# Kernel optimization log

Hardware: AMD Instinct MI355X
Metric: run time of the kernel (lower is better)

The kernel has to match this reference:

```python
import jax, jax.numpy as jnp
import numpy as np

B, T, V, D, OUT = 32, 100, 10000, 128, 1000
CODE_P = 0.003  # ~30 active codes per visit


def gru_dir(x3, whh, bhh, reverse):
    """x3: [B,T,3F] precomputed input-side gates (W_ih x + b_ih). PyTorch GRU math."""
    F = whh.shape[1]
    h0 = jnp.zeros((x3.shape[0], F), x3.dtype)

    def step(h, xt):
        gh = h @ whh.T + bhh
        xr, xz, xn = jnp.split(xt, 3, -1)
        hr, hz, hn = jnp.split(gh, 3, -1)
        r = jax.nn.sigmoid(xr + hr)
        z = jax.nn.sigmoid(xz + hz)
        n = jnp.tanh(xn + r * hn)
        h_new = (1.0 - z) * n + z * h
        return h_new, h_new

    _, hs = jax.lax.scan(step, h0, jnp.swapaxes(x3, 0, 1), reverse=reverse)
    return jnp.swapaxes(hs, 0, 1)  # [B,T,F]


def setup_inputs() -> dict:
    key = jax.random.key(0)
    ks = jax.random.split(key, 16)
    s = lambda k, *sh: jax.random.normal(k, sh, dtype=jnp.float32) * 0.05
    # multi-hot visits, ~0/1 with density CODE_P; force code 0 present so no all-zero visit
    x = (jax.random.uniform(ks[0], (B, T, V)) < CODE_P).astype(jnp.float32)
    x = x.at[:, :, 0].set(1.0)
    return {
        "batchdata": x,
        "emb": s(ks[1], V, D),
        "wih_f": s(ks[2], 3 * D, D), "whh_f": s(ks[3], 3 * D, D),
        "bih_f": jnp.zeros((3 * D,), jnp.float32), "bhh_f": jnp.zeros((3 * D,), jnp.float32),
        "wih_b": s(ks[4], 3 * D, D), "whh_b": s(ks[5], 3 * D, D),
        "bih_b": jnp.zeros((3 * D,), jnp.float32), "bhh_b": jnp.zeros((3 * D,), jnp.float32),
        "attn_w": s(ks[6], 2 * D, 1), "attn_b": jnp.zeros((1,), jnp.float32),
        "comb_w": s(ks[7], D, 4 * D), "comb_b": jnp.zeros((D,), jnp.float32),
        "fc_w": s(ks[8], OUT, D), "fc_b": jnp.zeros((OUT,), jnp.float32),
    }


def reference(batchdata, emb, wih_f, whh_f, bih_f, bhh_f, wih_b, whh_b, bih_b, bhh_b,
              attn_w, attn_b, comb_w, comb_b, fc_w, fc_b):
    # multihot_to_embedding: sum of embedding rows where visit==1 == multihot @ table
    e = jnp.einsum('btv,vd->btd', batchdata, emb)          # [B,T,D]
    mask = jnp.any(e != 0, axis=2)                          # [B,T]
    # DipoleLayer: bidirectional GRU (hidden=D each dir), dropout in eval mode = identity
    xf = jnp.einsum('btf,gf->btg', e, wih_f) + bih_f
    xb = jnp.einsum('btf,gf->btg', e, wih_b) + bih_b
    hf = gru_dir(xf, whh_f, bhh_f, reverse=False)
    hb = gru_dir(xb, whh_b, bhh_b, reverse=True)
    h = jnp.concatenate([hf, hb], axis=-1)                  # [B,T,2D]
    # location-based attention over timesteps
    scores = (h @ attn_w)[..., 0] + attn_b[0]               # [B,T]
    scores = jnp.where(mask, scores, jnp.float32(-1e9))
    a = jax.nn.softmax(scores, axis=-1)
    c = jnp.einsum('bt,btf->bf', a, h)                      # [B,2D] context
    last = jnp.sum(mask.astype(jnp.int32), axis=-1) - 1     # last valid visit
    h_last = h[jnp.arange(h.shape[0]), last]                # [B,2D]
    feat = jnp.tanh(jnp.concatenate([c, h_last], -1) @ comb_w.T + comb_b)  # [B,D]
    logits = feat @ fc_w.T + fc_b                           # [B,OUT]
    return logits
```

## Files before the change

### kernel.cpp

```cpp
#include <hip/hip_runtime.h>
#include <math.h>

#define BB 32
#define TT 100
#define VV 10000
#define DD 128
#define OUTN 1000
#define G3 384

__global__ __launch_bounds__(256) void k_embed(
    const float* __restrict__ x, const float* __restrict__ emb,
    float* __restrict__ e, int* __restrict__ mask)
{
    const int bt  = blockIdx.x;
    const int tid = threadIdx.x;
    __shared__ int   s_cnt;
    __shared__ int   s_any;
    __shared__ int   s_idx[256];
    __shared__ float s_val[256];
    if (tid == 0) { s_cnt = 0; s_any = 0; }
    __syncthreads();

    const float4* x4 = (const float4*)(x + (size_t)bt * VV);
    for (int i = tid; i < VV / 4; i += 256) {
        float4 v = x4[i];
        if (v.x != 0.f) { int p = atomicAdd(&s_cnt, 1); if (p < 256) { s_idx[p] = 4*i+0; s_val[p] = v.x; } }
        if (v.y != 0.f) { int p = atomicAdd(&s_cnt, 1); if (p < 256) { s_idx[p] = 4*i+1; s_val[p] = v.y; } }
        if (v.z != 0.f) { int p = atomicAdd(&s_cnt, 1); if (p < 256) { s_idx[p] = 4*i+2; s_val[p] = v.z; } }
        if (v.w != 0.f) { int p = atomicAdd(&s_cnt, 1); if (p < 256) { s_idx[p] = 4*i+3; s_val[p] = v.w; } }
    }
    __syncthreads();
    int cnt = s_cnt; if (cnt > 256) cnt = 256;
    if (tid < DD) {
        float acc = 0.f;
        for (int i = 0; i < cnt; ++i)
            acc += s_val[i] * emb[(size_t)s_idx[i] * DD + tid];
        e[(size_t)bt * DD + tid] = acc;
        if (acc != 0.f) s_any = 1;
    }
    __syncthreads();
    if (tid == 0) mask[bt] = s_any;
}

__global__ __launch_bounds__(256) void k_gates(
    const float* __restrict__ e,
    const float* __restrict__ wih_f, const float* __restrict__ bih_f,
    const float* __restrict__ wih_b, const float* __restrict__ bih_b,
    float* __restrict__ x3)
{
    const int r0  = blockIdx.x * 8;
    const int tid = threadIdx.x;
    __shared__ __align__(16) float se[8][DD];
    for (int i = tid; i < 8 * DD; i += 256)
        se[i >> 7][i & 127] = e[(size_t)(r0 + (i >> 7)) * DD + (i & 127)];
    __syncthreads();

    for (int cc = 0; cc < 3; ++cc) {
        const int col = tid + cc * 256;
        const float* wrow;
        float bias;
        if (col < G3) { wrow = wih_f + (size_t)col * DD;        bias = bih_f[col]; }
        else          { wrow = wih_b + (size_t)(col - G3) * DD; bias = bih_b[col - G3]; }
        float acc[8];
        #pragma unroll
        for (int r = 0; r < 8; ++r) acc[r] = 0.f;
        const float4* w4 = (const float4*)wrow;
        for (int k4 = 0; k4 < DD / 4; ++k4) {
            float4 w = w4[k4];
            #pragma unroll
            for (int r = 0; r < 8; ++r) {
                float4 ev = *(const float4*)&se[r][4 * k4];
                acc[r] += ev.x * w.x + ev.y * w.y + ev.z * w.z + ev.w * w.w;
            }
        }
        #pragma unroll
        for (int r = 0; r < 8; ++r)
            x3[(size_t)(r0 + r) * 768 + col] = acc[r] + bias;
    }
}

__global__ __launch_bounds__(384, 2) void k_gru(
    const float* __restrict__ x3,
    const float* __restrict__ whh_f, const float* __restrict__ bhh_f,
    const float* __restrict__ whh_b, const float* __restrict__ bhh_b,
    float* __restrict__ h_all)
{
    const int dir = blockIdx.x & 1;
    const int b   = blockIdx.x >> 1;
    const int g   = threadIdx.x;
    const float* whh = dir ? whh_b : whh_f;
    const float* bhh = dir ? bhh_b : bhh_f;

    float4 W[32];
    {
        const float4* wr4 = (const float4*)(whh + (size_t)g * DD);
        #pragma unroll
        for (int j = 0; j < 32; ++j) W[j] = wr4[j];
    }
    const float bh = bhh[g];

    __shared__ __align__(16) float h_lds[DD];
    __shared__ float gh_lds[G3];
    float h_reg = 0.f;
    if (g < DD) h_lds[g] = 0.f;
    __syncthreads();

    for (int t = 0; t < TT; ++t) {
        const int te = dir ? (TT - 1 - t) : t;
        const float* x3p = x3 + (size_t)(b * TT + te) * 768 + dir * G3;
        float xr = 0.f, xz = 0.f, xn = 0.f;
        if (g < DD) { xr = x3p[g]; xz = x3p[DD + g]; xn = x3p[2 * DD + g]; }

        float acc[8];
        #pragma unroll
        for (int i = 0; i < 8; ++i) acc[i] = 0.f;
        #pragma unroll
        for (int j = 0; j < 32; ++j) {
            float4 hv = *(const float4*)&h_lds[4 * j];
            float4 wv = W[j];
            acc[j & 7] += wv.x * hv.x + wv.y * hv.y + wv.z * hv.z + wv.w * hv.w;
        }
        gh_lds[g] = ((acc[0] + acc[1]) + (acc[2] + acc[3]))
                  + ((acc[4] + acc[5]) + (acc[6] + acc[7])) + bh;
        __syncthreads();

        if (g < DD) {
            float hr = gh_lds[g], hz = gh_lds[DD + g], hn = gh_lds[2 * DD + g];
            float r  = __builtin_amdgcn_rcpf(1.f + __expf(-(xr + hr)));
            float z  = __builtin_amdgcn_rcpf(1.f + __expf(-(xz + hz)));
            float e2 = __expf(2.f * (xn + r * hn));
            float n  = 1.f - 2.f * __builtin_amdgcn_rcpf(e2 + 1.f);
            float hnew = n + z * (h_reg - n);
            h_reg = hnew;
            h_lds[g] = hnew;
            h_all[(size_t)((dir * BB + b) * TT + te) * DD + g] = hnew;
        }
        __syncthreads();
    }
}

__global__ __launch_bounds__(256) void k_attn(
    const float* __restrict__ h_all, const int* __restrict__ mask,
    const float* __restrict__ attn_w, const float* __restrict__ attn_b,
    const float* __restrict__ comb_w, const float* __restrict__ comb_b,
    float* __restrict__ feat)
{
    const int b   = blockIdx.x;
    const int tid = threadIdx.x;
    __shared__ float s_aw[256];
    __shared__ float s_sc[128];
    __shared__ int   s_m[128];
    __shared__ float s_red[128];
    __shared__ __align__(16) float s_ch[512];

    s_aw[tid] = attn_w[tid];
    int m = 0;
    if (tid < 128) {
        m = (tid < TT) ? mask[b * TT + tid] : 0;
        s_m[tid] = m;
    }
    __syncthreads();
    for (int s = 64; s > 0; s >>= 1) {
        if (tid < s) s_m[tid] += s_m[tid + s];
        __syncthreads();
    }
    const int last = s_m[0] - 1;

    const float* hf = h_all + (size_t)(0 * BB + b) * TT * DD;
    const float* hb = h_all + (size_t)(1 * BB + b) * TT * DD;

    float sc = -1e9f;
    if (tid < TT) {
        float a = attn_b[0];
        const float4* hf4 = (const float4*)(hf + (size_t)tid * DD);
        const float4* hb4 = (const float4*)(hb + (size_t)tid * DD);
        for (int k = 0; k < DD / 4; ++k) {
            float4 v = hf4[k];
            a += v.x * s_aw[4*k] + v.y * s_aw[4*k+1] + v.z * s_aw[4*k+2] + v.w * s_aw[4*k+3];
        }
        for (int k = 0; k < DD / 4; ++k) {
            float4 v = hb4[k];
            a += v.x * s_aw[DD+4*k] + v.y * s_aw[DD+4*k+1] + v.z * s_aw[DD+4*k+2] + v.w * s_aw[DD+4*k+3];
        }
        sc = m ? a : -1e9f;
    }
    if (tid < 128) { s_sc[tid] = sc; s_red[tid] = sc; }
    __syncthreads();
    for (int s = 64; s > 0; s >>= 1) {
        if (tid < s) s_red[tid] = fmaxf(s_red[tid], s_red[tid + s]);
        __syncthreads();
    }
    const float mx = s_red[0];
    __syncthreads();
    float ex = 0.f;
    if (tid < 128) { ex = __expf(s_sc[tid] - mx); s_sc[tid] = ex; s_red[tid] = ex; }
    __syncthreads();
    for (int s = 64; s > 0; s >>= 1) {
        if (tid < s) s_red[tid] += s_red[tid + s];
        __syncthreads();
    }
    const float inv = 1.f / s_red[0];
    __syncthreads();

    {
        const int fl = tid & 127;
        const float* hp = (tid < 128) ? hf : hb;
        float csum = 0.f;
        for (int t = 0; t < TT; ++t)
            csum += s_sc[t] * hp[(size_t)t * DD + fl];
        s_ch[tid]       = csum * inv;
        s_ch[256 + tid] = hp[(size_t)last * DD + fl];
    }
    __syncthreads();

    if (tid < 128) {
        float a = comb_b[tid];
        const float4* cw = (const float4*)(comb_w + (size_t)tid * 512);
        for (int k = 0; k < 128; ++k) {
            float4 w4 = cw[k];
            float4 v4 = *(const float4*)&s_ch[4 * k];
            a += w4.x * v4.x + w4.y * v4.y + w4.z * v4.z + w4.w * v4.w;
        }
        feat[(size_t)b * DD + tid] = tanhf(a);
    }
}

__global__ __launch_bounds__(256) void k_logits(
    const float* __restrict__ feat, const float* __restrict__ fc_w,
    const float* __restrict__ fc_b, float* __restrict__ out)
{
    const int b   = blockIdx.x >> 2;
    const int oc  = blockIdx.x & 3;
    const int tid = threadIdx.x;
    const int o   = oc * 256 + tid;
    __shared__ __align__(16) float s_f[DD];
    if (tid < DD) s_f[tid] = feat[(size_t)b * DD + tid];
    __syncthreads();
    if (o < OUTN) {
        float a = fc_b[o];
        const float4* w4 = (const float4*)(fc_w + (size_t)o * DD);
        for (int k = 0; k < DD / 4; ++k) {
            float4 w = w4[k];
            float4 v = *(const float4*)&s_f[4 * k];
            a += w.x * v.x + w.y * v.y + w.z * v.z + w.w * v.w;
        }
        out[(size_t)b * OUTN + o] = a;
    }
}

extern "C" void kernel_launch(void* const* d_in, const int* in_sizes, int n_in,
                              void* d_out, int out_size, void* d_ws, size_t ws_size,
                              hipStream_t stream)
{
    const float* x      = (const float*)d_in[0];
    const float* emb    = (const float*)d_in[1];
    const float* wih_f  = (const float*)d_in[2];
    const float* whh_f  = (const float*)d_in[3];
    const float* bih_f  = (const float*)d_in[4];
    const float* bhh_f  = (const float*)d_in[5];
    const float* wih_b  = (const float*)d_in[6];
    const float* whh_b  = (const float*)d_in[7];
    const float* bih_b  = (const float*)d_in[8];
    const float* bhh_b  = (const float*)d_in[9];
    const float* attn_w = (const float*)d_in[10];
    const float* attn_b = (const float*)d_in[11];
    const float* comb_w = (const float*)d_in[12];
    const float* comb_b = (const float*)d_in[13];
    const float* fc_w   = (const float*)d_in[14];
    const float* fc_b   = (const float*)d_in[15];
    float* out = (float*)d_out;

    float* ws    = (float*)d_ws;
    float* e     = ws;
    int*   mask  = (int*)(ws + 409600);
    float* x3    = ws + 412800;
    float* h_all = ws + 2870400;
    float* feat  = ws + 3689600;

    k_embed <<<BB * TT,      256, 0, stream>>>(x, emb, e, mask);
    k_gates <<<(BB * TT)/8,  256, 0, stream>>>(e, wih_f, bih_f, wih_b, bih_b, x3);
    k_gru   <<<2 * BB,       384, 0, stream>>>(x3, whh_f, bhh_f, whh_b, bhh_b, h_all);
    k_attn  <<<BB,           256, 0, stream>>>(h_all, mask, attn_w, attn_b, comb_w, comb_b, feat);
    k_logits<<<BB * 4,       256, 0, stream>>>(feat, fc_w, fc_b, out);
}
```

Measured before the change: 414.4 us.

## Split GRU recurrent matvec by hidden unit and K-half across 256 threads

Reworks the GRU recurrence so each thread owns one hidden unit's r, z and n rows over half of the K dimension, instead of one thread per gate row. Each thread holds 48 float4 weights in registers. The upper half writes its partial sums to LDS and the lower half combines them and applies the gate math locally. This removes the gh_lds gather across gate rows and cuts the block to 256 threads, aiming to shorten the per-step critical path. The cost is higher register pressure (192 floats of weights per thread) and a cross-half partial-sum exchange each step.

```diff
diff --git a/kernel.cpp b/kernel.cpp
--- a/kernel.cpp
+++ b/kernel.cpp
@@ -79,7 +79,7 @@
     }
 }
 
-__global__ __launch_bounds__(384, 2) void k_gru(
+__global__ __launch_bounds__(256, 1) void k_gru(
     const float* __restrict__ x3,
     const float* __restrict__ whh_f, const float* __restrict__ bhh_f,
     const float* __restrict__ whh_b, const float* __restrict__ bhh_b,
@@ -87,45 +87,51 @@
 {
     const int dir = blockIdx.x & 1;
     const int b   = blockIdx.x >> 1;
-    const int g   = threadIdx.x;
+    const int tid = threadIdx.x;
+    const int g   = tid & 127;
+    const int kh  = tid >> 7;
+    const int kb  = kh * 64;
     const float* whh = dir ? whh_b : whh_f;
     const float* bhh = dir ? bhh_b : bhh_f;
 
-    float4 W[32];
-    {
-        const float4* wr4 = (const float4*)(whh + (size_t)g * DD);
-        #pragma unroll
-        for (int j = 0; j < 32; ++j) W[j] = wr4[j];
-    }
-    const float bh = bhh[g];
+    const float4* pr4 = (const float4*)(whh + (size_t)(g         ) * DD + kb);
+    const float4* pz4 = (const float4*)(whh + (size_t)(DD     + g) * DD + kb);
+    const float4* pn4 = (const float4*)(whh + (size_t)(2 * DD + g) * DD + kb);
+
+#define Q16(M) M(0) M(1) M(2) M(3) M(4) M(5) M(6) M(7) M(8) M(9) M(10) M(11) M(12) M(13) M(14) M(15)
+#define DECLW(i) float4 wr##i = pr4[i], wz##i = pz4[i], wn##i = pn4[i];
+    Q16(DECLW)
+
+    const float bhr = bhh[g], bhz = bhh[DD + g], bhn = bhh[2 * DD + g];
 
     __shared__ __align__(16) float h_lds[DD];
-    __shared__ float gh_lds[G3];
+    __shared__ float p_lds[3 * DD];
     float h_reg = 0.f;
-    if (g < DD) h_lds[g] = 0.f;
+    if (tid < DD) h_lds[tid] = 0.f;
     __syncthreads();
 
     for (int t = 0; t < TT; ++t) {
         const int te = dir ? (TT - 1 - t) : t;
         const float* x3p = x3 + (size_t)(b * TT + te) * 768 + dir * G3;
         float xr = 0.f, xz = 0.f, xn = 0.f;
-        if (g < DD) { xr = x3p[g]; xz = x3p[DD + g]; xn = x3p[2 * DD + g]; }
-
-        float acc[8];
-        #pragma unroll
-        for (int i = 0; i < 8; ++i) acc[i] = 0.f;
-        #pragma unroll
-        for (int j = 0; j < 32; ++j) {
-            float4 hv = *(const float4*)&h_lds[4 * j];
-            float4 wv = W[j];
-            acc[j & 7] += wv.x * hv.x + wv.y * hv.y + wv.z * hv.z + wv.w * hv.w;
-        }
-        gh_lds[g] = ((acc[0] + acc[1]) + (acc[2] + acc[3]))
-                  + ((acc[4] + acc[5]) + (acc[6] + acc[7])) + bh;
-        __syncthreads();
-
-        if (g < DD) {
-            float hr = gh_lds[g], hz = gh_lds[DD + g], hn = gh_lds[2 * DD + g];
+        if (tid < DD) { xr = x3p[g]; xz = x3p[DD + g]; xn = x3p[2 * DD + g]; }
+
+        float ar0 = 0.f, ar1 = 0.f, az0 = 0.f, az1 = 0.f, an0 = 0.f, an1 = 0.f;
+#define FMA(i) { float4 hv = *(const float4*)&h_lds[kb + 4 * (i)]; \
+        (((i)&1) ? ar1 : ar0) += wr##i.x*hv.x + wr##i.y*hv.y + wr##i.z*hv.z + wr##i.w*hv.w; \
+        (((i)&1) ? az1 : az0) += wz##i.x*hv.x + wz##i.y*hv.y + wz##i.z*hv.z + wz##i.w*hv.w; \
+        (((i)&1) ? an1 : an0) += wn##i.x*hv.x + wn##i.y*hv.y + wn##i.z*hv.z + wn##i.w*hv.w; }
+        Q16(FMA)
+#undef FMA
+        const float pr = ar0 + ar1, pz = az0 + az1, pn = an0 + an1;
+
+        if (kh) { p_lds[g] = pr; p_lds[DD + g] = pz; p_lds[2 * DD + g] = pn; }
+        __syncthreads();
+
+        if (tid < DD) {
+            float hr = pr + p_lds[g]          + bhr;
+            float hz = pz + p_lds[DD + g]     + bhz;
+            float hn = pn + p_lds[2 * DD + g] + bhn;
             float r  = __builtin_amdgcn_rcpf(1.f + __expf(-(xr + hr)));
             float z  = __builtin_amdgcn_rcpf(1.f + __expf(-(xz + hz)));
             float e2 = __expf(2.f * (xn + r * hn));
@@ -137,6 +143,8 @@
         }
         __syncthreads();
     }
+#undef DECLW
+#undef Q16
 }
 
 __global__ __launch_bounds__(256) void k_attn(
@@ -279,7 +287,7 @@
 
     k_embed <<<BB * TT,      256, 0, stream>>>(x, emb, e, mask);
     k_gates <<<(BB * TT)/8,  256, 0, stream>>>(e, wih_f, bih_f, wih_b, bih_b, x3);
-    k_gru   <<<2 * BB,       384, 0, stream>>>(x3, whh_f, bhh_f, whh_b, bhh_b, h_all);
+    k_gru   <<<2 * BB,       256, 0, stream>>>(x3, whh_f, bhh_f, whh_b, bhh_b, h_all);
     k_attn  <<<BB,           256, 0, stream>>>(h_all, mask, attn_w, attn_b, comb_w, comb_b, feat);
     k_logits<<<BB * 4,       256, 0, stream>>>(feat, fc_w, fc_b, out);
 }
```

Measured after the change: 372.9 us. -10.0%, faster.
